# Kernel optimization log

Measured on AMD Instinct MI355X. Metric: run time of the kernel, lower is better.

Reference implementation:

```python
import jax, jax.numpy as jnp
import numpy as np

C = 512        # channels
H = 8          # num_heads
GN_ATTN = 32   # GroupNorm32 groups
GN_CONV = 8    # Conv1dBlock GroupNorm groups


def _mish(x):
    return x * jnp.tanh(jax.nn.softplus(x))


def _group_norm(x, w, b, groups, eps=1e-5):
    # x: (B, C, T); normalize per group over (C//groups, T) in fp32
    B, Cc, T = x.shape
    xf = x.astype(jnp.float32).reshape(B, groups, Cc // groups, T)
    mean = xf.mean(axis=(2, 3), keepdims=True)
    var = xf.var(axis=(2, 3), keepdims=True)
    xn = ((xf - mean) * jax.lax.rsqrt(var + eps)).reshape(B, Cc, T)
    return (xn * w[None, :, None] + b[None, :, None]).astype(x.dtype)


def _conv1d_same(x, w, b):
    # x: (B, Cin, T), w: (Cout, Cin, K)
    y = jax.lax.conv_general_dilated(
        x, w, window_strides=(1,), padding='SAME',
        dimension_numbers=('NCH', 'OIH', 'NCH'))
    return y + b[None, :, None]


def setup_inputs() -> dict:
    key = jax.random.key(0)
    ks = jax.random.split(key, 12)
    B, T = 8, 1024
    s_qkv = 1.0 / np.sqrt(C * 2)
    s_proj = 1.0 / np.sqrt(C * 4)
    return {
        'x':       jax.random.normal(ks[0], (B, C, T), jnp.float32),
        'gn_w':    jnp.ones((C,), jnp.float32),
        'gn_b':    jnp.zeros((C,), jnp.float32),
        'wqkv':    jax.random.normal(ks[1], (3 * C, C, 2), jnp.float32) * s_qkv,
        'bqkv':    jnp.zeros((3 * C,), jnp.float32),
        'gnq_w':   jnp.ones((3 * C,), jnp.float32),
        'gnq_b':   jnp.zeros((3 * C,), jnp.float32),
        'wproj':   jax.random.normal(ks[2], (C, C, 4), jnp.float32) * s_proj,
        'bproj':   jnp.zeros((C,), jnp.float32),
        'gnp_w':   jnp.ones((C,), jnp.float32),
        'gnp_b':   jnp.zeros((C,), jnp.float32),
    }


def _qkv_attention(qkv):
    # qkv: (B*H, 3*dh, T)
    ch = qkv.shape[1] // 3
    q, k, v = jnp.split(qkv, 3, axis=1)
    scale = 1.0 / np.sqrt(np.sqrt(ch))
    # (bh, t, s) full score matrix, softmax in fp32 as original
    weight = jnp.einsum('bct,bcs->bts', q * scale, k * scale)
    weight = jax.nn.softmax(weight.astype(jnp.float32), axis=-1).astype(weight.dtype)
    return jnp.einsum('bts,bcs->bct', weight, v)


def reference(x, gn_w, gn_b, wqkv, bqkv, gnq_w, gnq_b, wproj, bproj, gnp_w, gnp_b):
    B, Cc, T = x.shape
    # norm -> qkv Conv1dBlock (conv -> GN(8) -> Mish)
    h = _group_norm(x, gn_w, gn_b, GN_ATTN)
    qkv = _mish(_group_norm(_conv1d_same(h, wqkv, bqkv), gnq_w, gnq_b, GN_CONV))
    # heads: (B, 3C, T) -> (B*H, 3C/H, T)
    qkv = qkv.reshape(B * H, (3 * Cc) // H, T)
    a = _qkv_attention(qkv)                       # (B*H, C/H, T)
    a = a.reshape(B, Cc, T)
    # proj Conv1dBlock + residual
    h = _mish(_group_norm(_conv1d_same(a, wproj, bproj), gnp_w, gnp_b, GN_CONV))
    return x + h
```

## Files before the change

### kernel.cpp

```cpp
#include <hip/hip_runtime.h>
#include <hip/hip_bf16.h>
#include <math.h>

#define TID threadIdx.x

constexpr int Cc = 512, Tt = 1024, C3 = 1536;

typedef __attribute__((ext_vector_type(8))) __bf16 bf16x8;
typedef __attribute__((ext_vector_type(4))) float f32x4;

__device__ __forceinline__ void async16(const void* g, void* l) {
  __builtin_amdgcn_global_load_lds(
      (const __attribute__((address_space(1))) unsigned int*)g,
      (__attribute__((address_space(3))) unsigned int*)l, 16, 0, 0);
}

__device__ __forceinline__ unsigned int pack2bf(float a, float b) {
  __hip_bfloat162 h;
  h.x = __float2bfloat16(a);
  h.y = __float2bfloat16(b);
  return *reinterpret_cast<unsigned int*>(&h);
}

__device__ __forceinline__ float bf2f(unsigned short u) {
  unsigned int t = ((unsigned int)u) << 16;
  union { unsigned int i; float f; } c;
  c.i = t;
  return c.f;
}

__device__ __forceinline__ float exp2_hw(float x) {
  float r;
  asm("v_exp_f32 %0, %1" : "=v"(r) : "v"(x));
  return r;
}

__device__ __forceinline__ float mishf(float x) {
  float u = __expf(x);
  float n = u * (u + 2.f);
  float r = x * n * __builtin_amdgcn_rcpf(n + 2.f);
  return (x > 20.f) ? x : r;
}

__device__ __forceinline__ void blockReduce2(float& s, float& ss) {
  #pragma unroll
  for (int off = 32; off > 0; off >>= 1) {
    s  += __shfl_xor(s,  off);
    ss += __shfl_xor(ss, off);
  }
  __shared__ float ls[4], lss[4];
  int w = TID >> 6;
  if ((TID & 63) == 0) { ls[w] = s; lss[w] = ss; }
  __syncthreads();
  s  = ls[0] + ls[1] + ls[2] + ls[3];
  ss = lss[0] + lss[1] + lss[2] + lss[3];
}

__global__ void zero_stats(float* p) { p[TID] = 0.f; }

__global__ __launch_bounds__(256) void zero_pads(__hip_bfloat16* __restrict__ aT) {
  int idx = blockIdx.x * 256 + TID;
  int bb = idx >> 11;
  int task = idx & 2047;
  int prow = task >> 6;
  int col = (task & 63) * 8;
  int P = (prow < 16) ? prow : (1024 + prow);
  uint4 z = {0u, 0u, 0u, 0u};
  *reinterpret_cast<uint4*>(aT + ((size_t)bb * 1056 + P) * 512 + col) = z;
}

__global__ __launch_bounds__(256) void gn1_im2col(const float* __restrict__ x,
    const float* __restrict__ w, const float* __restrict__ bv,
    __hip_bfloat16* __restrict__ B1t) {
  __shared__ float hs[16][262];
  int blk = blockIdx.x, bb = blk >> 5, g = blk & 31;
  size_t base = ((size_t)bb * Cc + g * 16) * Tt;
  const float* xp = x + base;
  float s = 0.f, ss = 0.f;
  for (int i = TID * 4; i < 16 * Tt; i += 1024) {
    float4 v = *reinterpret_cast<const float4*>(xp + i);
    s  += v.x + v.y + v.z + v.w;
    ss += v.x * v.x + v.y * v.y + v.z * v.z + v.w * v.w;
  }
  blockReduce2(s, ss);
  float mean = s * (1.f / 16384.f);
  float rstd = rsqrtf(ss * (1.f / 16384.f) - mean * mean + 1e-5f);

  char* ob = reinterpret_cast<char*>(B1t + (size_t)bb * Tt * 1024 + g * 32);
  for (int tc = 0; tc < 4; ++tc) {
    int tbase = tc * 256;
    __syncthreads();
    for (int task = TID; task < 1024; task += 256) {
      int row = task >> 6, c4 = task & 63;
      int ch = g * 16 + row;
      float sw = w[ch] * rstd;
      float sb = bv[ch] - mean * sw;
      float4 v = *reinterpret_cast<const float4*>(xp + (size_t)row * Tt + tbase + c4 * 4);
      hs[row][c4 * 4 + 0] = v.x * sw + sb;
      hs[row][c4 * 4 + 1] = v.y * sw + sb;
      hs[row][c4 * 4 + 2] = v.z * sw + sb;
      hs[row][c4 * 4 + 3] = v.w * sw + sb;
    }
    if (TID < 16) {
      int row = TID, t = tbase + 256;
      float val = 0.f;
      if (t < Tt) {
        int ch = g * 16 + row;
        float sw = w[ch] * rstd;
        float sb = bv[ch] - mean * sw;
        val = xp[(size_t)row * Tt + t] * sw + sb;
      }
      hs[row][256] = val;
    }
    __syncthreads();
    for (int task = TID; task < 1024; task += 256) {
      int t = task >> 2, cj = task & 3;
      int ci = cj * 4;
      uint4 u;
      u.x = pack2bf(hs[ci + 0][t], hs[ci + 0][t + 1]);
      u.y = pack2bf(hs[ci + 1][t], hs[ci + 1][t + 1]);
      u.z = pack2bf(hs[ci + 2][t], hs[ci + 2][t + 1]);
      u.w = pack2bf(hs[ci + 3][t], hs[ci + 3][t + 1]);
      *reinterpret_cast<uint4*>(ob + ((size_t)(tbase + t) * 1024 + cj * 8) * 2) = u;
    }
  }
}

__global__ __launch_bounds__(256) void cast_bf16(const float* __restrict__ in,
    __hip_bfloat16* __restrict__ out, int n) {
  int i = (blockIdx.x * 256 + TID) * 4;
  if (i >= n) return;
  float4 v = *reinterpret_cast<const float4*>(in + i);
  *reinterpret_cast<unsigned int*>(out + i)     = pack2bf(v.x, v.y);
  *reinterpret_cast<unsigned int*>(out + i + 2) = pack2bf(v.z, v.w);
}

__global__ __launch_bounds__(256) void cast_wproj(const float* __restrict__ wp,
    __hip_bfloat16* __restrict__ A2) {
  int o = blockIdx.x;
  int ci = TID * 2;
  float4 v0 = *reinterpret_cast<const float4*>(wp + ((size_t)o * 512 + ci) * 4);
  float4 v1 = *reinterpret_cast<const float4*>(wp + ((size_t)o * 512 + ci + 1) * 4);
  const float* a0 = &v0.x;
  const float* a1 = &v1.x;
  #pragma unroll
  for (int j = 0; j < 4; ++j) {
    unsigned int u = pack2bf(a0[j], a1[j]);
    *reinterpret_cast<unsigned int*>(A2 + ((size_t)j * 512 + o) * 512 + ci) = u;
  }
}

__global__ __launch_bounds__(1024, 4) void gemm_bt11(const __hip_bfloat16* __restrict__ A,
    const __hip_bfloat16* __restrict__ Bt, const float* __restrict__ bias,
    __hip_bfloat16* __restrict__ Cout, float* __restrict__ statraw) {
  constexpr int K = 1024;
  constexpr int BUF = 56 * 1024;
  __shared__ __align__(16) char lds[2 * BUF];
  int bz = blockIdx.x & 7;
  int inner = blockIdx.x >> 3;
  int t0 = (inner & 3) * 256;
  int og = inner >> 2;
  int o0 = og * 192;
  int wave = TID >> 6, lane = TID & 63;
  int l4 = lane >> 4, r15 = lane & 15;
  int wm = wave >> 2, wn = wave & 3;
  const __hip_bfloat16* Ab = A + (size_t)o0 * K;
  const __hip_bfloat16* Bb = Bt + ((size_t)bz * 1024 + t0) * K;

  f32x4 acc[3][4];
  f32x4 zz = {0.f, 0.f, 0.f, 0.f};
  #pragma unroll
  for (int m = 0; m < 3; ++m)
    #pragma unroll
    for (int n = 0; n < 4; ++n) acc[m][n] = zz;

  auto stage = [&](int kt, int buf) {
    char* dst = lds + buf * BUF;
    #pragma unroll
    for (int c = 0; c < 4; ++c) {
      int ch = c * 16 + wave;
      if (ch < 56) {
        int kof;
        const __hip_bfloat16* src;
        if (ch < 24) {
          int row = (ch >> 1) * 16 + r15;
          kof = kt * 64 + (ch & 1) * 32 + l4 * 8;
          src = Ab + (size_t)row * K + kof;
        } else {
          int cb = ch - 24;
          int row = (cb >> 1) * 16 + r15;
          kof = kt * 64 + (cb & 1) * 32 + l4 * 8;
          src = Bb + (size_t)row * K + kof;
        }
        async16(src, dst + ch * 1024 + lane * 16);
      }
    }
  };

  stage(0, 0);
  __syncthreads();
  for (int kt = 0; kt < 16; ++kt) {
    if (kt + 1 < 16) stage(kt + 1, (kt + 1) & 1);
    char* cur = lds + (kt & 1) * BUF;
    #pragma unroll
    for (int kk = 0; kk < 2; ++kk) {
      bf16x8 af[3], bfr[4];
      #pragma unroll
      for (int m = 0; m < 3; ++m)
        af[m] = *reinterpret_cast<const bf16x8*>(cur + ((wm * 3 + m) * 2 + kk) * 1024 + lane * 16);
      #pragma unroll
      for (int n = 0; n < 4; ++n)
        bfr[n] = *reinterpret_cast<const bf16x8*>(cur + (24 + (wn * 4 + n) * 2 + kk) * 1024 + lane * 16);
      #pragma unroll
      for (int m = 0; m < 3; ++m)
        #pragma unroll
        for (int n = 0; n < 4; ++n)
          acc[m][n] = __builtin_amdgcn_mfma_f32_16x16x32_bf16(af[m], bfr[n], acc[m][n], 0, 0, 0);
    }
    __syncthreads();
  }

  float* sred = reinterpret_cast<float*>(lds);
  #pragma unroll
  for (int m = 0; m < 3; ++m) {
    float s = 0.f, ss2 = 0.f;
    #pragma unroll
    for (int n = 0; n < 4; ++n) {
      int ocol = t0 + (wn * 4 + n) * 16 + r15;
      #pragma unroll
      for (int r = 0; r < 4; ++r) {
        int orow = o0 + (wm * 3 + m) * 16 + l4 * 4 + r;
        float v = acc[m][n][r] + bias[orow];
        Cout[((size_t)bz * C3 + orow) * 1024 + ocol] = __float2bfloat16(v);
        s += v;
        ss2 += v * v;
      }
    }
    #pragma unroll
    for (int off = 1; off < 64; off <<= 1) {
      s   += __shfl_xor(s, off);
      ss2 += __shfl_xor(ss2, off);
    }
    if (lane == 0) {
      sred[(wave * 3 + m) * 2]     = s;
      sred[(wave * 3 + m) * 2 + 1] = ss2;
    }
  }
  __syncthreads();
  if (TID == 0) {
    float S = 0.f, SS = 0.f;
    #pragma unroll
    for (int slot = 0; slot < 48; ++slot) {
      S  += sred[slot * 2];
      SS += sred[slot * 2 + 1];
    }
    int g = bz * 8 + og;
    atomicAdd(&statraw[2 * g],     S);
    atomicAdd(&statraw[2 * g + 1], SS);
  }
}

__global__ __launch_bounds__(256) void gemm_c4b(const __hip_bfloat16* __restrict__ A2,
    const __hip_bfloat16* __restrict__ aT, const float* __restrict__ bias,
    float* __restrict__ Cout, float* __restrict__ statraw) {
  constexpr int BUF = 42 * 1024;
  __shared__ __align__(16) char lds[2 * BUF];
  int bz = blockIdx.x & 7;
  int inner = blockIdx.x >> 3;
  int t0 = (inner & 7) * 128;
  int o0 = (inner >> 3) * 128;
  int wave = TID >> 6, lane = TID & 63;
  int l4 = lane >> 4, r15 = lane & 15;
  int wm = wave >> 1, wn = wave & 1;
  const __hip_bfloat16* aTb = aT + (size_t)bz * 1056 * 512;

  f32x4 acc[4][4];
  f32x4 zz = {0.f, 0.f, 0.f, 0.f};
  #pragma unroll
  for (int m = 0; m < 4; ++m)
    #pragma unroll
    for (int n = 0; n < 4; ++n) acc[m][n] = zz;

  auto stage = [&](int kt, int buf) {
    char* dst = lds + buf * BUF;
    #pragma unroll
    for (int c = 0; c < 11; ++c) {
      int ch = c * 4 + wave;
      if (ch < 42) {
        const __hip_bfloat16* src;
        if (ch < 32) {
          int j = ch >> 3, rg = ch & 7;
          src = A2 + ((size_t)j * 512 + o0 + rg * 16 + r15) * 512 + kt * 32 + l4 * 8;
        } else {
          int rg = ch - 32;
          src = aTb + (size_t)(t0 + rg * 16 + r15) * 512 + kt * 32 + l4 * 8;
        }
        async16(src, dst + ch * 1024 + lane * 16);
      }
    }
  };

  stage(0, 0);
  __syncthreads();
  for (int kt = 0; kt < 16; ++kt) {
    if (kt + 1 < 16) stage(kt + 1, (kt + 1) & 1);
    char* cur = lds + (kt & 1) * BUF;
    #pragma unroll
    for (int j = 0; j < 4; ++j) {
      bf16x8 af[4], bfr[4];
      #pragma unroll
      for (int m = 0; m < 4; ++m)
        af[m] = *reinterpret_cast<const bf16x8*>(cur + (j * 8 + wm * 4 + m) * 1024 + lane * 16);
      #pragma unroll
      for (int n = 0; n < 4; ++n) {
        int q = (wn * 4 + n) * 16 + r15 + j + 15;
        bfr[n] = *reinterpret_cast<const bf16x8*>(cur + 32 * 1024 + (q >> 4) * 1024 + l4 * 256 + (q & 15) * 16);
      }
      #pragma unroll
      for (int m = 0; m < 4; ++m)
        #pragma unroll
        for (int n = 0; n < 4; ++n)
          acc[m][n] = __builtin_amdgcn_mfma_f32_16x16x32_bf16(af[m], bfr[n], acc[m][n], 0, 0, 0);
    }
    __syncthreads();
  }

  float* sred = reinterpret_cast<float*>(lds);
  #pragma unroll
  for (int m = 0; m < 4; ++m) {
    float s = 0.f, ss2 = 0.f;
    #pragma unroll
    for (int n = 0; n < 4; ++n) {
      int ocol = t0 + (wn * 4 + n) * 16 + r15;
      #pragma unroll
      for (int r = 0; r < 4; ++r) {
        int orow = o0 + (wm * 4 + m) * 16 + l4 * 4 + r;
        float v = acc[m][n][r] + bias[orow];
        Cout[((size_t)bz * Cc + orow) * 1024 + ocol] = v;
        s += v;
        ss2 += v * v;
      }
    }
    #pragma unroll
    for (int off = 1; off < 64; off <<= 1) {
      s   += __shfl_xor(s, off);
      ss2 += __shfl_xor(ss2, off);
    }
    if (lane == 0) {
      sred[(wave * 4 + m) * 2]     = s;
      sred[(wave * 4 + m) * 2 + 1] = ss2;
    }
  }
  __syncthreads();
  if (TID < 2) {
    int g0 = o0 >> 6;
    float S = 0.f, SS = 0.f;
    int cnt = 0;
    #pragma unroll
    for (int slot = 0; slot < 16; ++slot) {
      int rc = ((slot >> 3) << 2) + (slot & 3);
      int g = (o0 + rc * 16) >> 6;
      if (g == g0 + (int)TID) {
        S  += sred[slot * 2];
        SS += sred[slot * 2 + 1];
        ++cnt;
      }
    }
    if (cnt) {
      atomicAdd(&statraw[2 * (bz * 8 + g0 + TID)],     S);
      atomicAdd(&statraw[2 * (bz * 8 + g0 + TID) + 1], SS);
    }
  }
}

__global__ __launch_bounds__(256) void gn2_prep(const __hip_bfloat16* __restrict__ qkv,
    const float* __restrict__ straw, const float* __restrict__ w, const float* __restrict__ bv,
    char* __restrict__ qTp, char* __restrict__ kimg, char* __restrict__ vimg) {
  __shared__ unsigned short hbf[192 * 66];
  int tl = blockIdx.x & 15, hb = blockIdx.x >> 4;
  int b = hb >> 3, hd = hb & 7;
  float rs = straw[2 * (b * 8 + hd)], rq = straw[2 * (b * 8 + hd) + 1];
  float mean = rs * (1.f / 196608.f);
  float rstd = rsqrtf(fmaxf(rq * (1.f / 196608.f) - mean * mean, 0.f) + 1e-5f);
  for (int task = TID; task < 768; task += 256) {
    int row = task >> 2, seg = task & 3;
    int ch = hd * 192 + row;
    float sw = w[ch] * rstd;
    float sb = bv[ch] - mean * sw;
    const uint4* src = reinterpret_cast<const uint4*>(
        qkv + ((size_t)(b * C3 + ch)) * 1024 + tl * 64 + seg * 16);
    uint4 u0 = src[0], u1 = src[1];
    unsigned int uu[8] = {u0.x, u0.y, u0.z, u0.w, u1.x, u1.y, u1.z, u1.w};
    unsigned int* dst = reinterpret_cast<unsigned int*>(&hbf[row * 66 + seg * 16]);
    #pragma unroll
    for (int j = 0; j < 8; ++j) {
      float a = mishf(bf2f((unsigned short)(uu[j] & 0xffff)) * sw + sb);
      float c = mishf(bf2f((unsigned short)(uu[j] >> 16)) * sw + sb);
      dst[j] = pack2bf(a, c);
    }
  }
  __syncthreads();
  size_t tileof = ((size_t)hb * 16 + tl) * 8192;
  {
    int t = TID & 63, sel = TID >> 6;
    int img = sel >> 1, half = sel & 1;
    char* obase = (img == 0 ? qTp : kimg) + tileof + (size_t)t * 128;
    #pragma unroll
    for (int cc = 0; cc < 4; ++cc) {
      int chunk = half * 4 + cc;
      uint4 u;
      unsigned int* up = reinterpret_cast<unsigned int*>(&u);
      #pragma unroll
      for (int j = 0; j < 4; ++j) {
        int c = chunk * 8 + j * 2;
        unsigned int lo = hbf[(img * 64 + c) * 66 + t];
        unsigned int hi = hbf[(img * 64 + c + 1) * 66 + t];
        up[j] = lo | (hi << 16);
      }
      int cpos = (img == 0) ? chunk : (chunk ^ (t & 7));
      *reinterpret_cast<uint4*>(obase + cpos * 16) = u;
    }
  }
  {
    int c = TID & 63, qtr = TID >> 6;
    const unsigned int* vrow = reinterpret_cast<const unsigned int*>(&hbf[(128 + c) * 66]);
    char* obase = vimg + tileof + (size_t)c * 128;
    #pragma unroll
    for (int k = 0; k < 2; ++k) {
      int chunk = qtr * 2 + k;
      uint4 u;
      unsigned int* up = reinterpret_cast<unsigned int*>(&u);
      #pragma unroll
      for (int j = 0; j < 4; ++j) up[j] = vrow[chunk * 4 + j];
      *reinterpret_cast<uint4*>(obase + (chunk ^ (c & 7)) * 16) = u;
    }
  }
}

__global__ __launch_bounds__(1024) void attn_mfma6(const char* __restrict__ qTp,
    const char* __restrict__ kimg, const char* __restrict__ vimg,
    __hip_bfloat16* __restrict__ aT) {
  __shared__ __align__(16) char smem[131072];
  char* kbuf0 = smem;
  char* kbuf1 = smem + 16384;
  char* vbuf0 = smem + 32768;
  char* vbuf1 = smem + 49152;
  char* pp    = smem + 65536;
  char* ov    = smem;

  int hb = blockIdx.y;
  int b = hb >> 3, hd = hb & 7;
  int lane = TID & 63, wave = TID >> 6;
  int qt = wave >> 2, qw = wave & 3;
  int l4 = lane >> 4, r15 = lane & 15;
  size_t ibase = (size_t)hb * 16 * 8192;
  const char* ksrc = kimg + ibase;
  const char* vsrc = vimg + ibase;

  async16(ksrc + (size_t)TID * 16, kbuf0 + (size_t)TID * 16);
  async16(vsrc + (size_t)TID * 16, vbuf0 + (size_t)TID * 16);

  bf16x8 aq[2];
  int tg = qw * 16 + r15;
  const char* qrow = qTp + ibase + (size_t)(blockIdx.x * 4 + qt) * 8192 + (size_t)tg * 128;
  aq[0] = *reinterpret_cast<const bf16x8*>(qrow + l4 * 16);
  aq[1] = *reinterpret_cast<const bf16x8*>(qrow + 64 + l4 * 16);
  {
    const float SC = 0.125f * 1.44269504f;
    #pragma unroll
    for (int kk = 0; kk < 2; ++kk) {
      unsigned int* u = reinterpret_cast<unsigned int*>(&aq[kk]);
      #pragma unroll
      for (int j = 0; j < 4; ++j) {
        float lo = bf2f((unsigned short)(u[j] & 0xffff)) * SC;
        float hi = bf2f((unsigned short)(u[j] >> 16)) * SC;
        u[j] = pack2bf(lo, hi);
      }
    }
  }

  f32x4 osum[4];
  f32x4 zz = {0.f, 0.f, 0.f, 0.f};
  #pragma unroll
  for (int cf = 0; cf < 4; ++cf) osum[cf] = zz;
  float mrow[4] = {-1e30f, -1e30f, -1e30f, -1e30f};
  float lrow[4] = {0.f, 0.f, 0.f, 0.f};
  __syncthreads();

  for (int it = 0; it < 8; ++it) {
    char* kcur = (it & 1) ? kbuf1 : kbuf0;
    char* vcur = (it & 1) ? vbuf1 : vbuf0;
    if (it < 7) {
      char* knxt = (it & 1) ? kbuf0 : kbuf1;
      char* vnxt = (it & 1) ? vbuf0 : vbuf1;
      const char* kn = ksrc + (size_t)(it + 1) * 16384;
      const char* vn = vsrc + (size_t)(it + 1) * 16384;
      async16(kn + (size_t)TID * 16, knxt + (size_t)TID * 16);
      async16(vn + (size_t)TID * 16, vnxt + (size_t)TID * 16);
    }
    f32x4 sc[8];
    #pragma unroll
    for (int sf = 0; sf < 8; ++sf) sc[sf] = zz;
    #pragma unroll
    for (int sf = 0; sf < 8; ++sf) {
      int sr = sf * 16 + r15;
      #pragma unroll
      for (int kk = 0; kk < 2; ++kk) {
        bf16x8 bk = *reinterpret_cast<const bf16x8*>(kcur + sr * 128 + (((kk * 4 + l4) ^ (sr & 7)) << 4));
        sc[sf] = __builtin_amdgcn_mfma_f32_16x16x32_bf16(aq[kk], bk, sc[sf], 0, 0, 0);
      }
    }
    float tmax[4];
    #pragma unroll
    for (int r = 0; r < 4; ++r) {
      float m0 = fmaxf(fmaxf(sc[0][r], sc[1][r]), fmaxf(sc[2][r], sc[3][r]));
      float m1 = fmaxf(fmaxf(sc[4][r], sc[5][r]), fmaxf(sc[6][r], sc[7][r]));
      tmax[r] = fmaxf(m0, m1);
    }
    #pragma unroll
    for (int off = 1; off < 16; off <<= 1)
      #pragma unroll
      for (int r = 0; r < 4; ++r) tmax[r] = fmaxf(tmax[r], __shfl_xor(tmax[r], off));
    bool grow = (tmax[0] > mrow[0]) | (tmax[1] > mrow[1]) |
                (tmax[2] > mrow[2]) | (tmax[3] > mrow[3]);
    if (grow) {
      float alpha[4];
      #pragma unroll
      for (int r = 0; r < 4; ++r) {
        float mnew = fmaxf(mrow[r], tmax[r]);
        alpha[r] = exp2_hw(mrow[r] - mnew);
        mrow[r] = mnew;
        lrow[r] *= alpha[r];
      }
      #pragma unroll
      for (int cf = 0; cf < 4; ++cf)
        #pragma unroll
        for (int r = 0; r < 4; ++r) osum[cf][r] *= alpha[r];
    }
    char* pw = pp + wave * 4096;
    float psum[4] = {0.f, 0.f, 0.f, 0.f};
    #pragma unroll
    for (int sf = 0; sf < 8; ++sf) {
      int s = sf * 16 + r15;
      int chunk = s >> 3;
      #pragma unroll
      for (int r = 0; r < 4; ++r) {
        float p = exp2_hw(sc[sf][r] - mrow[r]);
        psum[r] += p;
        int tlc = l4 * 4 + r;
        *reinterpret_cast<__hip_bfloat16*>(pw + tlc * 256 + (((chunk ^ (tlc & 15)) << 4) | ((s & 7) * 2)))
            = __float2bfloat16(p);
      }
    }
    #pragma unroll
    for (int r = 0; r < 4; ++r) lrow[r] += psum[r];
    asm volatile("s_waitcnt lgkmcnt(0)" ::: "memory");
    __builtin_amdgcn_sched_barrier(0);

    bf16x8 pa[4];
    #pragma unroll
    for (int kk2 = 0; kk2 < 4; ++kk2)
      pa[kk2] = *reinterpret_cast<const bf16x8*>(pw + r15 * 256 + (((kk2 * 4 + l4) ^ (r15 & 15)) << 4));
    #pragma unroll
    for (int cf = 0; cf < 4; ++cf) {
      int cr = cf * 16 + r15;
      #pragma unroll
      for (int kk2 = 0; kk2 < 4; ++kk2) {
        bf16x8 bv = *reinterpret_cast<const bf16x8*>(vcur + (kk2 >> 1) * 8192 + cr * 128 +
                                                     ((((kk2 & 1) * 4 + l4) ^ (cr & 7)) << 4));
        osum[cf] = __builtin_amdgcn_mfma_f32_16x16x32_bf16(pa[kk2], bv, osum[cf], 0, 0, 0);
      }
    }
    __syncthreads();
  }

  #pragma unroll
  for (int off = 1; off < 16; off <<= 1)
    #pragma unroll
    for (int r = 0; r < 4; ++r) lrow[r] += __shfl_xor(lrow[r], off);
  float linv[4];
  #pragma unroll
  for (int r = 0; r < 4; ++r) linv[r] = 1.f / lrow[r];

  #pragma unroll
  for (int cf = 0; cf < 4; ++cf) {
    int c = cf * 16 + r15;
    #pragma unroll
    for (int r = 0; r < 4; ++r) {
      int t = qt * 64 + qw * 16 + l4 * 4 + r;
      *reinterpret_cast<__hip_bfloat16*>(ov + t * 128 + ((((c >> 3) ^ (t & 7)) << 4) | ((c & 7) * 2)))
          = __float2bfloat16(osum[cf][r] * linv[r]);
    }
  }
  __syncthreads();
  __hip_bfloat16* ap = aT + ((size_t)b * 1056 + 16 + blockIdx.x * 256) * 512 + hd * 64;
  for (int u = TID; u < 2048; u += 1024) {
    int t = u >> 3, cj = u & 7;
    uint4 o4 = *reinterpret_cast<const uint4*>(ov + t * 128 + ((cj ^ (t & 7)) << 4));
    *reinterpret_cast<uint4*>(ap + (size_t)t * 512 + cj * 8) = o4;
  }
}

__global__ __launch_bounds__(256) void final_kernel(const float* __restrict__ x,
    float* __restrict__ y, const float* __restrict__ straw,
    const float* __restrict__ w, const float* __restrict__ bv) {
  size_t i = ((size_t)blockIdx.x * 256 + TID) * 4;
  int ch = (int)((i >> 10) & (Cc - 1));
  int b = (int)(i >> 19);
  int g = b * 8 + (ch >> 6);
  float rs = straw[2 * g], rq = straw[2 * g + 1];
  float mean = rs * (1.f / 65536.f);
  float rstd = rsqrtf(fmaxf(rq * (1.f / 65536.f) - mean * mean, 0.f) + 1e-5f);
  float sw = w[ch] * rstd;
  float sb = bv[ch] - mean * sw;
  float4 v  = *reinterpret_cast<const float4*>(y + i);
  float4 xv = *reinterpret_cast<const float4*>(x + i);
  v.x = xv.x + mishf(v.x * sw + sb);
  v.y = xv.y + mishf(v.y * sw + sb);
  v.z = xv.z + mishf(v.z * sw + sb);
  v.w = xv.w + mishf(v.w * sw + sb);
  *reinterpret_cast<float4*>(y + i) = v;
}

extern "C" void kernel_launch(void* const* d_in, const int* in_sizes, int n_in,
                              void* d_out, int out_size, void* d_ws, size_t ws_size,
                              hipStream_t stream) {
  const float* x     = (const float*)d_in[0];
  const float* gn_w  = (const float*)d_in[1];
  const float* gn_b  = (const float*)d_in[2];
  const float* wqkv  = (const float*)d_in[3];
  const float* bqkv  = (const float*)d_in[4];
  const float* gnq_w = (const float*)d_in[5];
  const float* gnq_b = (const float*)d_in[6];
  const float* wproj = (const float*)d_in[7];
  const float* bproj = (const float*)d_in[8];
  const float* gnp_w = (const float*)d_in[9];
  const float* gnp_b = (const float*)d_in[10];
  float* out = (float*)d_out;

  char* ws = (char*)d_ws;
  const size_t MB = 1024 * 1024;
  __hip_bfloat16* qkvb = (__hip_bfloat16*)ws;
  __hip_bfloat16* aT   = (__hip_bfloat16*)(ws + 24 * MB);
  __hip_bfloat16* A1   = (__hip_bfloat16*)(ws + 56 * MB);
  char* vimg = ws + 56 * MB;
  __hip_bfloat16* A2   = (__hip_bfloat16*)(ws + 56 * MB);
  float* st2raw = (float*)(ws + 64 * MB);
  float* st3raw = st2raw + 128;
  __hip_bfloat16* B1t = (__hip_bfloat16*)d_out;
  char* qTp  = (char*)d_out;
  char* kimg = (char*)d_out + 8 * MB;

  dim3 blk(256);
  zero_stats<<<1, blk, 0, stream>>>(st2raw);
  zero_pads<<<64, blk, 0, stream>>>(aT);
  cast_bf16<<<1536, blk, 0, stream>>>(wqkv, A1, C3 * 1024);
  gn1_im2col<<<256, blk, 0, stream>>>(x, gn_w, gn_b, B1t);
  gemm_bt11<<<256, dim3(1024), 0, stream>>>(A1, B1t, bqkv, qkvb, st2raw);
  gn2_prep<<<1024, blk, 0, stream>>>(qkvb, st2raw, gnq_w, gnq_b, qTp, kimg, vimg);
  attn_mfma6<<<dim3(4, 64), dim3(1024), 0, stream>>>(qTp, kimg, vimg, aT);
  cast_wproj<<<512, blk, 0, stream>>>(wproj, A2);
  gemm_c4b<<<256, blk, 0, stream>>>(A2, aT, bproj, out, st3raw);
  final_kernel<<<4096, blk, 0, stream>>>(x, out, st3raw, gnp_w, gnp_b);
}
```

Before: 162.1 us.

## Replace im2col qkv conv GEMM with shifted-row reuse of padded transposed activations

Stops materialising a K=1024 im2col matrix for the kernel-size-2 qkv convolution. Instead, GN1 output is written once as a padded (T+pad, C) bf16 image, and the two conv taps are split into separate weight slices. The GEMM stages a 17-row-group tile of activations per k-step and reads it at row offsets 0 and +1 from LDS for the two taps. This halves the activation staging traffic and LDS footprint per stage, at the cost of an extra pad-zeroing launch and more complex, possibly bank-conflicting LDS addressing.

```diff
diff --git a/kernel.cpp b/kernel.cpp
--- a/kernel.cpp
+++ b/kernel.cpp
@@ -69,9 +69,9 @@
   *reinterpret_cast<uint4*>(aT + ((size_t)bb * 1056 + P) * 512 + col) = z;
 }
 
-__global__ __launch_bounds__(256) void gn1_im2col(const float* __restrict__ x,
+__global__ __launch_bounds__(256) void gn1_hT(const float* __restrict__ x,
     const float* __restrict__ w, const float* __restrict__ bv,
-    __hip_bfloat16* __restrict__ B1t) {
+    __hip_bfloat16* __restrict__ hT) {
   __shared__ float hs[16][262];
   int blk = blockIdx.x, bb = blk >> 5, g = blk & 31;
   size_t base = ((size_t)bb * Cc + g * 16) * Tt;
@@ -86,7 +86,7 @@
   float mean = s * (1.f / 16384.f);
   float rstd = rsqrtf(ss * (1.f / 16384.f) - mean * mean + 1e-5f);
 
-  char* ob = reinterpret_cast<char*>(B1t + (size_t)bb * Tt * 1024 + g * 32);
+  __hip_bfloat16* ob = hT + (size_t)bb * 1056 * 512 + g * 16;
   for (int tc = 0; tc < 4; ++tc) {
     int tbase = tc * 256;
     __syncthreads();
@@ -101,38 +101,29 @@
       hs[row][c4 * 4 + 2] = v.z * sw + sb;
       hs[row][c4 * 4 + 3] = v.w * sw + sb;
     }
-    if (TID < 16) {
-      int row = TID, t = tbase + 256;
-      float val = 0.f;
-      if (t < Tt) {
-        int ch = g * 16 + row;
-        float sw = w[ch] * rstd;
-        float sb = bv[ch] - mean * sw;
-        val = xp[(size_t)row * Tt + t] * sw + sb;
-      }
-      hs[row][256] = val;
-    }
     __syncthreads();
-    for (int task = TID; task < 1024; task += 256) {
-      int t = task >> 2, cj = task & 3;
-      int ci = cj * 4;
+    for (int task = TID; task < 512; task += 256) {
+      int t = task >> 1, half = task & 1;
+      int c0 = half * 8;
       uint4 u;
-      u.x = pack2bf(hs[ci + 0][t], hs[ci + 0][t + 1]);
-      u.y = pack2bf(hs[ci + 1][t], hs[ci + 1][t + 1]);
-      u.z = pack2bf(hs[ci + 2][t], hs[ci + 2][t + 1]);
-      u.w = pack2bf(hs[ci + 3][t], hs[ci + 3][t + 1]);
-      *reinterpret_cast<uint4*>(ob + ((size_t)(tbase + t) * 1024 + cj * 8) * 2) = u;
-    }
-  }
-}
-
-__global__ __launch_bounds__(256) void cast_bf16(const float* __restrict__ in,
-    __hip_bfloat16* __restrict__ out, int n) {
-  int i = (blockIdx.x * 256 + TID) * 4;
-  if (i >= n) return;
-  float4 v = *reinterpret_cast<const float4*>(in + i);
-  *reinterpret_cast<unsigned int*>(out + i)     = pack2bf(v.x, v.y);
-  *reinterpret_cast<unsigned int*>(out + i + 2) = pack2bf(v.z, v.w);
+      u.x = pack2bf(hs[c0 + 0][t], hs[c0 + 1][t]);
+      u.y = pack2bf(hs[c0 + 2][t], hs[c0 + 3][t]);
+      u.z = pack2bf(hs[c0 + 4][t], hs[c0 + 5][t]);
+      u.w = pack2bf(hs[c0 + 6][t], hs[c0 + 7][t]);
+      *reinterpret_cast<uint4*>(ob + (size_t)(16 + tbase + t) * 512 + c0) = u;
+    }
+  }
+}
+
+__global__ __launch_bounds__(256) void cast_wqkv(const float* __restrict__ wq,
+    __hip_bfloat16* __restrict__ A1s) {
+  int o = blockIdx.x;
+  int ci = TID * 2;
+  float4 v = *reinterpret_cast<const float4*>(wq + ((size_t)o * 512 + ci) * 2);
+  unsigned int u0 = pack2bf(v.x, v.z);
+  unsigned int u1 = pack2bf(v.y, v.w);
+  *reinterpret_cast<unsigned int*>(A1s + (size_t)o * 512 + ci) = u0;
+  *reinterpret_cast<unsigned int*>(A1s + ((size_t)1536 + o) * 512 + ci) = u1;
 }
 
 __global__ __launch_bounds__(256) void cast_wproj(const float* __restrict__ wp,
@@ -150,11 +141,10 @@
   }
 }
 
-__global__ __launch_bounds__(1024, 4) void gemm_bt11(const __hip_bfloat16* __restrict__ A,
-    const __hip_bfloat16* __restrict__ Bt, const float* __restrict__ bias,
+__global__ __launch_bounds__(1024, 4) void gemm_s2(const __hip_bfloat16* __restrict__ A1s,
+    const __hip_bfloat16* __restrict__ hT, const float* __restrict__ bias,
     __hip_bfloat16* __restrict__ Cout, float* __restrict__ statraw) {
-  constexpr int K = 1024;
-  constexpr int BUF = 56 * 1024;
+  constexpr int BUF = 41 * 1024;
   __shared__ __align__(16) char lds[2 * BUF];
   int bz = blockIdx.x & 7;
   int inner = blockIdx.x >> 3;
@@ -164,8 +154,7 @@
   int wave = TID >> 6, lane = TID & 63;
   int l4 = lane >> 4, r15 = lane & 15;
   int wm = wave >> 2, wn = wave & 3;
-  const __hip_bfloat16* Ab = A + (size_t)o0 * K;
-  const __hip_bfloat16* Bb = Bt + ((size_t)bz * 1024 + t0) * K;
+  const __hip_bfloat16* hTb = hT + (size_t)bz * 1056 * 512;
 
   f32x4 acc[3][4];
   f32x4 zz = {0.f, 0.f, 0.f, 0.f};
@@ -177,20 +166,17 @@
   auto stage = [&](int kt, int buf) {
     char* dst = lds + buf * BUF;
     #pragma unroll
-    for (int c = 0; c < 4; ++c) {
+    for (int c = 0; c < 3; ++c) {
       int ch = c * 16 + wave;
-      if (ch < 56) {
-        int kof;
+      if (ch < 41) {
         const __hip_bfloat16* src;
         if (ch < 24) {
-          int row = (ch >> 1) * 16 + r15;
-          kof = kt * 64 + (ch & 1) * 32 + l4 * 8;
-          src = Ab + (size_t)row * K + kof;
+          int j = (ch >= 12) ? 1 : 0;
+          int rg = ch - j * 12;
+          src = A1s + ((size_t)j * 1536 + o0 + rg * 16 + r15) * 512 + kt * 32 + l4 * 8;
         } else {
-          int cb = ch - 24;
-          int row = (cb >> 1) * 16 + r15;
-          kof = kt * 64 + (cb & 1) * 32 + l4 * 8;
-          src = Bb + (size_t)row * K + kof;
+          int rg = ch - 24;
+          src = hTb + (size_t)(16 + t0 + rg * 16 + r15) * 512 + kt * 32 + l4 * 8;
         }
         async16(src, dst + ch * 1024 + lane * 16);
       }
@@ -203,14 +189,16 @@
     if (kt + 1 < 16) stage(kt + 1, (kt + 1) & 1);
     char* cur = lds + (kt & 1) * BUF;
     #pragma unroll
-    for (int kk = 0; kk < 2; ++kk) {
+    for (int j = 0; j < 2; ++j) {
       bf16x8 af[3], bfr[4];
       #pragma unroll
       for (int m = 0; m < 3; ++m)
-        af[m] = *reinterpret_cast<const bf16x8*>(cur + ((wm * 3 + m) * 2 + kk) * 1024 + lane * 16);
-      #pragma unroll
-      for (int n = 0; n < 4; ++n)
-        bfr[n] = *reinterpret_cast<const bf16x8*>(cur + (24 + (wn * 4 + n) * 2 + kk) * 1024 + lane * 16);
+        af[m] = *reinterpret_cast<const bf16x8*>(cur + (j * 12 + wm * 3 + m) * 1024 + lane * 16);
+      #pragma unroll
+      for (int n = 0; n < 4; ++n) {
+        int q = (wn * 4 + n) * 16 + r15 + j;
+        bfr[n] = *reinterpret_cast<const bf16x8*>(cur + 24 * 1024 + (q >> 4) * 1024 + l4 * 256 + (q & 15) * 16);
+      }
       #pragma unroll
       for (int m = 0; m < 3; ++m)
         #pragma unroll
@@ -642,21 +630,22 @@
   const size_t MB = 1024 * 1024;
   __hip_bfloat16* qkvb = (__hip_bfloat16*)ws;
   __hip_bfloat16* aT   = (__hip_bfloat16*)(ws + 24 * MB);
-  __hip_bfloat16* A1   = (__hip_bfloat16*)(ws + 56 * MB);
+  __hip_bfloat16* A1s  = (__hip_bfloat16*)(ws + 40 * MB);
+  __hip_bfloat16* A2   = (__hip_bfloat16*)(ws + 44 * MB);
   char* vimg = ws + 56 * MB;
-  __hip_bfloat16* A2   = (__hip_bfloat16*)(ws + 56 * MB);
   float* st2raw = (float*)(ws + 64 * MB);
   float* st3raw = st2raw + 128;
-  __hip_bfloat16* B1t = (__hip_bfloat16*)d_out;
+  __hip_bfloat16* hT = (__hip_bfloat16*)d_out;
   char* qTp  = (char*)d_out;
   char* kimg = (char*)d_out + 8 * MB;
 
   dim3 blk(256);
   zero_stats<<<1, blk, 0, stream>>>(st2raw);
   zero_pads<<<64, blk, 0, stream>>>(aT);
-  cast_bf16<<<1536, blk, 0, stream>>>(wqkv, A1, C3 * 1024);
-  gn1_im2col<<<256, blk, 0, stream>>>(x, gn_w, gn_b, B1t);
-  gemm_bt11<<<256, dim3(1024), 0, stream>>>(A1, B1t, bqkv, qkvb, st2raw);
+  zero_pads<<<64, blk, 0, stream>>>(hT);
+  cast_wqkv<<<1536, blk, 0, stream>>>(wqkv, A1s);
+  gn1_hT<<<256, blk, 0, stream>>>(x, gn_w, gn_b, hT);
+  gemm_s2<<<256, dim3(1024), 0, stream>>>(A1s, hT, bqkv, qkvb, st2raw);
   gn2_prep<<<1024, blk, 0, stream>>>(qkvb, st2raw, gnq_w, gnq_b, qTp, kimg, vimg);
   attn_mfma6<<<dim3(4, 64), dim3(1024), 0, stream>>>(qTp, kimg, vimg, aT);
   cast_wproj<<<512, blk, 0, stream>>>(wproj, A2);
```

After: 155.5 us. 1.04x faster.
